# Performance work log

Measured on AMD Instinct MI355X. Metric: run time of the kernel, lower is better.

Reference implementation:

```python
import jax, jax.numpy as jnp
import numpy as np
from jax.scipy.linalg import expm

J = 1.0
TEMP = 2.269
D = 28
RGSTEP = 12
TORDER = (1, 2, 3, 0)


def _plan():
    # statically trace tensor shapes through the RG steps
    shapes, d0s, dcuts = [], [], []
    t = (2, 2, 2, 2)
    for _ in range(RGSTEP):
        n = t[0] * t[0]          # antisymmetric matrix A_i is (n, n)
        dcut = min(D, t[2] * t[2])
        shapes.append(n)
        d0s.append(t[0])
        dcuts.append(dcut)
        # T1 = (dcut, t[1], dcut, t[3]); rotate by (1,2,3,0)
        t = (t[1], dcut, t[3], dcut)
    return shapes, d0s, dcuts

SHAPES, D0S, DCUTS = _plan()
OFFS = np.cumsum([0] + [n * (n - 1) // 2 for n in SHAPES])
TRIU = [np.triu_indices(n, k=1) for n in SHAPES]


def setup_inputs() -> dict:
    key = jax.random.key(0)
    # Ising initial tensor (initT): entries 0.5*sqrt(W_i W_j W_k W_l) for even parity
    beta = -J / TEMP
    W = np.array([np.exp(beta) + np.exp(-beta), np.exp(beta) - np.exp(-beta)])
    idx = np.indices((2, 2, 2, 2))
    par = (idx.sum(0) % 2) == 0
    prod = W[idx[0]] * W[idx[1]] * W[idx[2]] * W[idx[3]]
    T0 = np.where(par, 0.5 * np.sqrt(np.where(par, prod, 1.0)), 0.0)
    Aflat = jax.random.normal(key, (int(OFFS[-1]),), dtype=jnp.float32) * 0.05
    return {"Aflat": Aflat, "T0": jnp.asarray(T0, jnp.float32)}


def _build_Us(Aflat):
    Us = []
    for i in range(RGSTEP):
        n = SHAPES[i]
        seg = Aflat[int(OFFS[i]):int(OFFS[i + 1])]
        r, c = TRIU[i]
        A = jnp.zeros((n, n), Aflat.dtype).at[r, c].set(seg).at[c, r].set(-seg)
        U = expm(A)[:, :DCUTS[i]].reshape(D0S[i], D0S[i], DCUTS[i])
        Us.append(U)
    return Us


def _contract(T, U):
    # T1[a,b,c,e] = sum_{i,j,m,n,p} U[i,j,a] T[i,b,m,n] T[j,n,p,e] U[m,p,c]
    X = jnp.einsum('ija,ibmn->jbmna', U, T)   # O(D^6), peak D^5 intermediate
    Y = jnp.einsum('jbmna,jnpe->bmpea', X, T)  # O(D^7)
    return jnp.einsum('bmpea,mpc->abce', Y, U)  # O(D^6)


def reference(Aflat, T0):
    Us = _build_Us(Aflat)
    T = T0
    fe = jnp.zeros((), T0.dtype)
    for i in range(RGSTEP):
        T1 = _contract(T, Us[i])
        lam = jnp.max(jnp.abs(T1))
        T = jnp.transpose(T1 / lam, TORDER)
        fe = fe - TEMP * jnp.log(lam) / (2.0 ** (i + 1))
    return fe
```

## Files before the change

kernel.cpp:

```cpp
#include <hip/hip_runtime.h>


#define TEMPC 2.269f

typedef unsigned int uint32;
typedef short short8b __attribute__((ext_vector_type(8)));
typedef float f32x4 __attribute__((ext_vector_type(4)));
typedef unsigned short ushort8v __attribute__((ext_vector_type(8)));

__device__ __forceinline__ ushort f2bf(float x) {
  uint32 u = __float_as_uint(x);
  u = (u + 0x7FFFu + ((u >> 16) & 1u)) >> 16;
  return (ushort)u;
}
__device__ __forceinline__ float toF(float x) { return x; }
__device__ __forceinline__ float toF(ushort h) { return __uint_as_float(((uint32)h) << 16); }

__device__ __forceinline__ void gll16(const ushort* g, ushort* l) {
  __builtin_amdgcn_global_load_lds((const __attribute__((address_space(1))) void*)g,
                                   (__attribute__((address_space(3))) void*)l, 16, 0, 0);
}

template<int BM, int BN, bool PD>
__global__ __launch_bounds__(256) void gemm_mfma(
// ... 64 lines not shown
      int rr = li >> 3, ch = li & 7;
      int sch = ch ^ (rr & 7);
      if (isA) {
        if (PD) gll16(A + (long)pdBase[t] + (long)(k0 >> npl) * dsp, &As[tt * 512]);
        else    gll16(Ap + (long)rr * Kp + k0 + sch * 8, &As[tt * 512]);
      } else {
        gll16(Bp + (long)rr * Kp + k0 + sch * 8, &Bs[tt * 512]);
      }
    }
    __syncthreads();
    #pragma unroll
    for (int km = 0; km < 2; ++km) {
      short8b af[FRM], bfv[FRN];
      #pragma unroll
      for (int i = 0; i < FRM; ++i) {
        int rr = wm0 + i * 16 + rl;
        af[i] = *(const short8b*)&As[rr * 64 + ((((km << 2) | cb) ^ (rr & 7)) << 3)];
      }
      #pragma unroll
      for (int j = 0; j < FRN; ++j) {
        int rr = wn0 + j * 16 + rl;
        bfv[j] = *(const short8b*)&Bs[rr * 64 + ((((km << 2) | cb) ^ (rr & 7)) << 3)];
      }
      #pragma unroll
      for (int i = 0; i < FRM; ++i)
        #pragma unroll
        for (int j = 0; j < FRN; ++j)
          acc[i][j] = __builtin_amdgcn_mfma_f32_16x16x32_bf16(af[i], bfv[j], acc[i][j], 0, 0, 0);
    }
    __syncthreads();
  }
  const int r4 = (lane >> 4) * 4, cl = lane & 15;
  #pragma unroll
  for (int i = 0; i < FRM; ++i) {
    #pragma unroll
    for (int j = 0; j < FRN; ++j) {
      int row0 = m0 + wm0 + i * 16 + r4;
      int col  = n0 + wn0 + j * 16 + cl;
      #pragma unroll
      for (int qq = 0; qq < 4; ++qq) {
        long off2 = (long)bz * sC + (long)(row0 + qq) * Np + col;
        float v = acc[i][j][qq];
        if (mode & 1) v += cA * Aadd[off2] + ((row0 + qq) == col ? cI : 0.0f);
        if (mode & 2) Cf[off2] = v;
        if (mode & 4) Cb[off2] = f2bf(v);
      }
    }
  }
}

template<typename TI>
__global__ __launch_bounds__(256) void trans_to_bfT(const TI* __restrict__ in, ushort* __restrict__ out,
                                                    int R, int C, int inStride, int outStride, int Rpad,
                                                    long sIn, long sOut)
{
  __shared__ float sm[32][33];
  const TI* ip = in + (long)blockIdx.z * sIn;
  ushort* op = out + (long)blockIdx.z * sOut;
  int c0 = blockIdx.x * 32, r0 = blockIdx.y * 32;
  int lx = threadIdx.x & 31, ly = threadIdx.x >> 5;
  #pragma unroll
  for (int yy = 0; yy < 4; ++yy) {
    int r = r0 + ly + yy * 8, c = c0 + lx;
    if (r < R && c < C) sm[ly + yy * 8][lx] = toF(ip[(long)r * inStride + c]);
  }
  __syncthreads();
  #pragma unroll
  for (int yy = 0; yy < 4; ++yy) {
    int orow = c0 + ly + yy * 8;
    int ocol = r0 + lx;
    if (orow < C && ocol < Rpad) {
      ushort v = 0;
      if (ocol < R) v = f2bf(sm[lx][ly + yy * 8]);
      op[(long)orow * outStride + ocol] = v;
    }
  }
}

template<typename TT>
__global__ __launch_bounds__(256) void transTk2(const TT* __restrict__ T, ushort* __restrict__ out,
                                                int d0, int t3, int npl, long R1, long R1p)
{
  long idx = (long)blockIdx.x * 256 + threadIdx.x;
  if (idx >= R1p * 64) return;
  long rp = idx >> 6; int ii = (int)(idx & 63);
  long bm = rp >> npl; int n = (int)(rp & ((1 << npl) - 1));
  ushort v = 0;
  if (ii < d0 && n < t3) v = f2bf(toF(T[(long)ii * R1 + bm * t3 + n]));
  out[idx] = v;
}

template<typename TI>
__global__ __launch_bounds__(256) void build_B2(const TI* __restrict__ in, ushort* __restrict__ out,
                                                int t2, int t3, int d0, int npl, int Kp2, int Nr)
{
  __shared__ float sm[32][33];
  const int npad = 1 << npl;
  int oc0 = blockIdx.x * 32, or0 = blockIdx.y * 32;
  int lx = threadIdx.x & 31, ly = threadIdx.x >> 5;
  #pragma unroll
  for (int yy = 0; yy < 4; ++yy) {
    int ocol = oc0 + ly + yy * 8;
    int orow = or0 + lx;
    float v = 0.f;
    int j = ocol >> npl, n = ocol & (npad - 1);
    if (n < t3 && orow < Nr && j < d0) {
      int p = orow / t3, e = orow - p * t3;
      v = toF(in[((long)(j * t3 + n) * t2 + p) * t3 + e]);
    }
    sm[ly + yy * 8][lx] = v;
  }
  __syncthreads();
  #pragma unroll
  for (int yy = 0; yy < 4; ++yy) {
    int orow = or0 + ly + yy * 8;
    int ocol = oc0 + lx;
    if (orow < Nr) out[(long)orow * Kp2 + ocol] = f2bf(sm[lx][ly + yy * 8]);
  }
}

__global__ __launch_bounds__(256) void build_ut1(const float* __restrict__ U, ushort* __restrict__ out,
                                                 int d0, int dc, int Mpad, long uStr, long oStr)
{
  const int bt = blockIdx.y;
  int idx = blockIdx.x * 256 + threadIdx.x;
  if (idx >= Mpad * 64) return;
  int ja = idx >> 6, ii = idx & 63;
  ushort v = 0;
  if (ii < d0 && ja < d0 * dc) {
    int j = ja / dc, a = ja - j * dc;
    v = f2bf(U[bt * uStr + ((long)ii * d0 + j) * dc + a]);
  }
  out[bt * oStr + idx] = v;
}

__global__ __launch_bounds__(256) void build_ut3(const float* __restrict__ U, ushort* __restrict__ out,
                                                 int d0, int dc, int Kp3, long uStr, long oStr)
{
  const int bt = blockIdx.y;
  int idx = blockIdx.x * 256 + threadIdx.x;
  if (idx >= 64 * Kp3) return;
  int c = idx / Kp3, mp = idx - c * Kp3;
  ushort v = 0;
  if (c < dc && mp < d0 * d0) v = f2bf(U[bt * uStr + (long)mp * dc + c]);
  out[bt * oStr + idx] = v;
}

template<int KPG>
__global__ __launch_bounds__(256) void k3_fused(
    const ushort* __restrict__ Y, const ushort* __restrict__ Ut3,
    float* __restrict__ Z2, unsigned* __restrict__ lamslot,
    int d0, int t2, int t3, int dc, int NpY)
{
  __shared__ __align__(16) ushort sYt[32 * KPG];
  const int tid = threadIdx.x;
  const int wid = tid >> 6, lane = tid & 63;
  const int b = blockIdx.x / dc, a = blockIdx.x - b * dc;
  for (int i8 = tid; i8 < 32 * KPG / 8; i8 += 256) *(ushort8v*)&sYt[i8 * 8] = ushort8v{};
  __syncthreads();
  const int nv = NpY / 8;
  for (int idx = tid; idx < t2 * nv; idx += 256) {
    int m = idx / nv, v = idx - m * nv;
    int col0 = v * 8;
    ushort8v val = *(const ushort8v*)(Y + ((long)(b * t2 + m) * dc + a) * NpY + col0);
    #pragma unroll
    for (int u = 0; u < 8; ++u) {
      int col = col0 + u;
      int p = (t3 == 16) ? (col >> 4) : ((col * 9363) >> 18);
      if (p < t2) {
        int e = col - p * t3;
        int k = m * d0 + p;
        sYt[e * KPG + ((((k >> 3) ^ (e & 7)) << 3) | (k & 7))] = val[u];
      }
    }
  }
  __syncthreads();
  const int kpw = KPG / 4, k0w = wid * kpw;
  const int rl = lane & 15, cb = lane >> 4;
  f32x4 acc[2][2];
  #pragma unroll
  for (int i = 0; i < 2; ++i)
    #pragma unroll
    for (int j = 0; j < 2; ++j) { acc[i][j][0]=0.f; acc[i][j][1]=0.f; acc[i][j][2]=0.f; acc[i][j][3]=0.f; }
  for (int kk = 0; kk < kpw; kk += 32) {
    int kb = k0w + kk + cb * 8;
    short8b af[2], bfv[2];
    #pragma unroll
    for (int i = 0; i < 2; ++i) {
      int e = i * 16 + rl;
      af[i] = *(const short8b*)&sYt[e * KPG + (((kb >> 3) ^ (e & 7)) << 3)];
      bfv[i] = *(const short8b*)(Ut3 + (long)(i * 16 + rl) * KPG + kb);
    }
    #pragma unroll
    for (int i = 0; i < 2; ++i)
      #pragma unroll
      for (int j = 0; j < 2; ++j)
        acc[i][j] = __builtin_amdgcn_mfma_f32_16x16x32_bf16(af[i], bfv[j], acc[i][j], 0, 0, 0);
  }
  __syncthreads();
  float* Lp = (float*)sYt;
  #pragma unroll
  for (int i = 0; i < 2; ++i)
    #pragma unroll
    for (int j = 0; j < 2; ++j)
      #pragma unroll
      for (int qq = 0; qq < 4; ++qq) {
        int e32 = i * 16 + (lane >> 4) * 4 + qq;
        int c32 = j * 16 + (lane & 15);
        Lp[wid * 1024 + e32 * 32 + c32] = acc[i][j][qq];
      }
  __syncthreads();
  float mx = 0.f;
  for (int idx = tid; idx < 1024; idx += 256) {
    float z = Lp[idx] + Lp[1024 + idx] + Lp[2048 + idx] + Lp[3072 + idx];
    int e = idx >> 5, c = idx & 31;
    if (e < t3 && c < dc) {
      Z2[((long)(b * dc + a) * t3 + e) * 64 + c] = z;
      mx = fmaxf(mx, fabsf(z));
    }
  }
  __syncthreads();
  Lp[tid] = mx;
  __syncthreads();
  for (int s = 128; s > 0; s >>= 1) {
    if (tid < s) Lp[tid] = fmaxf(Lp[tid], Lp[tid + s]);
    __syncthreads();
  }
  if (tid == 0) atomicMax(lamslot, __float_as_uint(Lp[0]));
}

__global__ __launch_bounds__(256) void permute_scale2d(const float* __restrict__ Z2, ushort* __restrict__ Tn,
                                                       const unsigned* __restrict__ lamslot,
                                                       float* __restrict__ fe, float w, float* __restrict__ dout,
                                                       int dc, int t3)
{
  extern __shared__ char dynC[];
  ushort* sm = (ushort*)dynC;
  const int b = blockIdx.x;
  const int c0 = blockIdx.y * 7;
  const int tid = threadIdx.x;
  const float lam = __uint_as_float(*lamslot);
  const float s = 1.0f / lam;
  if (b == 0 && blockIdx.y == 0 && tid == 0) {
    float f = fe[0] - w * logf(lam);
    fe[0] = f; dout[0] = f;
  }
  const int TD = t3 * dc;
  const int tot = dc * t3 * 7;
  for (int idx = tid; idx < tot; idx += 256) {
    int c7 = idx % 7; int rm = idx / 7;
    int e = rm % t3; int a = rm / t3;
    float v = Z2[(((long)(b * dc + a)) * t3 + e) * 64 + c0 + c7] * s;
    sm[(c7 * t3 + e) * dc + a] = f2bf(v);
  }
  __syncthreads();
  const long ob = (long)(b * dc + c0) * TD;
  for (int idx = tid; idx < tot / 8; idx += 256)
    *(ushort8v*)(Tn + ob + idx * 8) = *(ushort8v*)(sm + idx * 8);
}

__global__ __launch_bounds__(256) void build_A2(const float* __restrict__ Aflat, float* __restrict__ Af,
                                                ushort* __restrict__ Ab, ushort* __restrict__ An,
                                                int n, int Np, long aoff, long tri, float sc)
{
  const int b = blockIdx.y;
  const long nn = (long)Np * Np;
  const long id = (long)blockIdx.x * 256 + threadIdx.x;
  if (id >= nn) return;
  const int r = (int)(id / Np), c = (int)(id % Np);
  float v = 0.0f;
  if (r < n && c < n) {
    if (c > r)      v =  Aflat[aoff + b * tri + (long)r * (n - 1) - (long)r * (r - 1) / 2 + (c - r - 1)] * sc;
    else if (c < r) v = -Aflat[aoff + b * tri + (long)c * (n - 1) - (long)c * (c - 1) / 2 + (r - c - 1)] * sc;
  }
  long o = b * nn + id;
  Af[o] = v; Ab[o] = f2bf(v); An[o] = f2bf(-v);
}

__global__ __launch_bounds__(256) void axpy_q2(const ushort* __restrict__ A2b, const float* __restrict__ Af,
                                               ushort* __restrict__ Qb, int Np)
{
  const int b = blockIdx.y;
  const long nn = (long)Np * Np;
  const long id = (long)blockIdx.x * 256 + threadIdx.x;
  if (id >= nn) return;
  const int r = (int)(id / Np), c = (int)(id % Np);
  long o = b * nn + id;
  float v = (1.0f/40320.0f) * toF(A2b[o]) + (1.0f/5040.0f) * Af[o] + ((r == c) ? (1.0f/720.0f) : 0.0f);
  Qb[o] = f2bf(v);
}

__global__ __launch_bounds__(256) void extract_u2(const float* __restrict__ E, float* __restrict__ W,
                                                  int n, int dcut, int rowStride, long ubase, long ustride, long estride)
{
  const int b = blockIdx.y;
  const long tot = (long)n * dcut;
  const long id = (long)blockIdx.x * 256 + threadIdx.x;
  if (id >= tot) return;
  const int rr = (int)(id / dcut), aa = (int)(id % dcut);
  W[ubase + b * ustride + id] = E[b * estride + (long)rr * rowStride + aa];
}

struct SmallStep { int n, d0, dcut, s; long aoff; long uoff; };
struct SmallStep4 { SmallStep st[4]; };

__global__ __launch_bounds__(256) void expm_small_kernel(const float* __restrict__ Aflat,
                                                         float* __restrict__ W, SmallStep4 ps)
{
  SmallStep p = ps.st[blockIdx.x];
  const int n = p.n, nn = n * n;
  __shared__ float As[256], A2[256], Qa[256], Qb[256];
  const int tid = threadIdx.x;
  const int r = (tid < nn) ? (tid / n) : 0;
  const int c = (tid < nn) ? (tid % n) : 0;
  const float sc = 1.0f / (float)(1 << p.s);
  if (tid < nn) {
    float v = 0.0f;
    if (c > r)      v =  Aflat[p.aoff + (long)r*(n-1) - (long)r*(r-1)/2 + (c - r - 1)] * sc;
    else if (c < r) v = -Aflat[p.aoff + (long)c*(n-1) - (long)c*(c-1)/2 + (r - c - 1)] * sc;
    As[tid] = v;
  }
  __syncthreads();
  if (tid < nn) {
    float s2 = 0.0f;
    for (int k = 0; k < n; ++k) s2 += As[r*n+k] * As[k*n+c];
    A2[tid] = s2;
  }
  __syncthreads();
  if (tid < nn)
    Qa[tid] = (1.0f/40320.0f)*A2[tid] + (1.0f/5040.0f)*As[tid] + ((r==c) ? (1.0f/720.0f) : 0.0f);
  __syncthreads();
  float* qp = Qa; float* qn = Qb;
  const float cis[3] = {1.0f/24.0f, 0.5f, 1.0f};
  const float cas[3] = {1.0f/120.0f, 1.0f/6.0f, 1.0f};
  #pragma unroll
  for (int it = 0; it < 3; ++it) {
    if (tid < nn) {
      float s2 = 0.0f;
      for (int k = 0; k < n; ++k) s2 += A2[r*n+k] * qp[k*n+c];
      qn[tid] = s2 + cas[it]*As[tid] + ((r==c) ? cis[it] : 0.0f);
    }
    __syncthreads();
    float* t = qp; qp = qn; qn = t;
  }
  for (int it = 0; it < p.s; ++it) {
    float s2 = 0.0f;
    if (tid < nn) { for (int k = 0; k < n; ++k) s2 += qp[r*n+k] * qp[k*n+c]; }
    if (tid < nn) qn[tid] = s2;
    __syncthreads();
    float* t = qp; qp = qn; qn = t;
  }
  if (tid < n * p.dcut) {
    int rr = tid / p.dcut, aa = tid % p.dcut;
    W[p.uoff + tid] = qp[rr*n + aa];
  }
}

template<int BM, int BN, int BK, int TM, int TN>
__global__ __launch_bounds__(256) void gemm_f32(
    const float* __restrict__ A, const float* __restrict__ B, float* __restrict__ C,
    int M, int N, int K)
{
  constexpr int PAD = 4;
  __shared__ float As[BK][BM + PAD];
  __shared__ float Bs[BK][BN + PAD];
  const int tid = threadIdx.x;
  const int m0 = blockIdx.y * BM, n0 = blockIdx.x * BN;
  constexpr int TX = BN / TN;
  const int tx = tid % TX, ty = tid / TX;
  float acc[TM][TN];
  #pragma unroll
  for (int i = 0; i < TM; ++i)
    #pragma unroll
    for (int j = 0; j < TN; ++j) acc[i][j] = 0.0f;

  const int a_m = tid / (BK / 4);
  const int a_k = (tid % (BK / 4)) * 4;
  const int b_k = tid / (BN / 4);
  const int b_n = (tid % (BN / 4)) * 4;

  for (int k0 = 0; k0 < K; k0 += BK) {
    float4 av = make_float4(0.f, 0.f, 0.f, 0.f);
    if (m0 + a_m < M && k0 + a_k < K)
      av = *(const float4*)(A + (long)(m0 + a_m) * K + k0 + a_k);
    As[a_k + 0][a_m] = av.x; As[a_k + 1][a_m] = av.y;
    As[a_k + 2][a_m] = av.z; As[a_k + 3][a_m] = av.w;
    float4 bv = make_float4(0.f, 0.f, 0.f, 0.f);
    if (k0 + b_k < K && n0 + b_n < N)
      bv = *(const float4*)(B + (long)(k0 + b_k) * N + n0 + b_n);
    *(float4*)&Bs[b_k][b_n] = bv;
    __syncthreads();
    #pragma unroll
    for (int kk = 0; kk < BK; ++kk) {
      float af[TM], bf[TN];
      #pragma unroll
      for (int i = 0; i < TM; i += 4) *(float4*)&af[i] = *(const float4*)&As[kk][ty*TM + i];
      #pragma unroll
      for (int j = 0; j < TN; j += 4) *(float4*)&bf[j] = *(const float4*)&Bs[kk][tx*TN + j];
      #pragma unroll
      for (int i = 0; i < TM; ++i)
        #pragma unroll
        for (int j = 0; j < TN; ++j)
          acc[i][j] = fmaf(af[i], bf[j], acc[i][j]);
    }
    __syncthreads();
  }
  #pragma unroll
  for (int i = 0; i < TM; ++i) {
    int row = m0 + ty*TM + i;
    if (row >= M) continue;
    #pragma unroll
    for (int j = 0; j < TN; ++j) {
      int col = n0 + tx*TN + j;
      if (col >= N) continue;
      C[(long)row * N + col] = acc[i][j];
    }
  }
}

__global__ __launch_bounds__(256) void k1_kernel2(const float* __restrict__ T, const float* __restrict__ U,
                                                  float* __restrict__ X2f,
                                                  int t1, int t2, int t3, int d0, int dcut, int K)
{
  extern __shared__ char dyn3[];
  float* lds = (float*)dyn3;
  float* Ts = lds;
  float* Us = lds + d0 * t3;
  const int tid = threadIdx.x;
  const int bm = blockIdx.x;
  const long tstride = (long)t1 * t2 * t3;
  const long tbase = (long)bm * t3;
  for (int idx = tid; idx < d0 * t3; idx += 256) {
    int i = idx / t3, nn = idx % t3;
    Ts[idx] = T[(long)i * tstride + tbase + nn];
  }
  const int nout = dcut * t3;
  __syncthreads();
  for (int j = 0; j < d0; ++j) {
    for (int idx = tid; idx < d0 * dcut; idx += 256)
      Us[idx] = U[((long)(idx / dcut) * d0 + j) * dcut + (idx % dcut)];
    __syncthreads();
    for (int idx = tid; idx < nout; idx += 256) {
      int a = idx / t3, nn = idx % t3;
      float s = 0.0f;
      for (int i = 0; i < d0; ++i) s += Ts[i*t3 + nn] * Us[i*dcut + a];
      X2f[((long)bm * dcut + a) * K + j * t3 + nn] = s;
    }
    __syncthreads();
  }
}

__global__ __launch_bounds__(256) void k3_kernel2(const float* __restrict__ Y, const float* __restrict__ U,
                                                  float* __restrict__ Z, int t1, int t2, int t3, int d0, int dcut,
                                                  int Ystride)
{
  extern __shared__ char dyn4[];
  float* lds = (float*)dyn4;
  float* Ys = lds;
  float* Us = lds + d0 * t3;
  const int tid = threadIdx.x;
  const int ba = blockIdx.x;
  const int b = ba / dcut, a = ba % dcut;
  const int nout = dcut * t3;
  float acc[4] = {0.f, 0.f, 0.f, 0.f};
  for (int m = 0; m < t2; ++m) {
    const long yrow = ((long)(b*t2 + m) * dcut + a) * Ystride;
    for (int idx = tid; idx < d0 * t3; idx += 256) Ys[idx] = Y[yrow + idx];
    for (int idx = tid; idx < d0 * dcut; idx += 256) Us[idx] = U[(long)m * d0 * dcut + idx];
    __syncthreads();
    #pragma unroll
    for (int o = 0; o < 4; ++o) {
      int idx = tid + o * 256;
      if (idx < nout) {
        int cc = idx / t3, e = idx % t3;
        float s = 0.0f;
        for (int p = 0; p < d0; ++p) s += Ys[p*t3 + e] * Us[p*dcut + cc];
        acc[o] += s;
      }
    }
    __syncthreads();
  }
  #pragma unroll
  for (int o = 0; o < 4; ++o) {
    int idx = tid + o * 256;
    if (idx < nout) {
      int cc = idx / t3, e = idx % t3;
      Z[(((long)a * t1 + b) * dcut + cc) * t3 + e] = acc[o];
    }
  }
}

__global__ __launch_bounds__(256) void redmax1_kernel(const float* __restrict__ Z, long cnt, float* __restrict__ part)
{
  __shared__ float sm[256];
  float v = 0.0f;
  for (long i = (long)blockIdx.x * 256 + threadIdx.x; i < cnt; i += (long)gridDim.x * 256)
    v = fmaxf(v, fabsf(Z[i]));
  sm[threadIdx.x] = v; __syncthreads();
  for (int s = 128; s > 0; s >>= 1) {
    if ((int)threadIdx.x < s) sm[threadIdx.x] = fmaxf(sm[threadIdx.x], sm[threadIdx.x + s]);
    __syncthreads();
  }
  if (threadIdx.x == 0) part[blockIdx.x] = sm[0];
}

__global__ __launch_bounds__(256) void redmax2_kernel(const float* __restrict__ part, float* __restrict__ invlam,
                                                      float* __restrict__ fe, float w, float* __restrict__ dout)
{
  __shared__ float sm[256];
  sm[threadIdx.x] = part[threadIdx.x]; __syncthreads();
  for (int s = 128; s > 0; s >>= 1) {
    if ((int)threadIdx.x < s) sm[threadIdx.x] = fmaxf(sm[threadIdx.x], sm[threadIdx.x + s]);
    __syncthreads();
  }
  if (threadIdx.x == 0) {
    float lam = sm[0];
    invlam[0] = 1.0f / lam;
    float f = fe[0] - w * logf(lam);
    fe[0] = f;
    dout[0] = f;
  }
}

__global__ __launch_bounds__(256) void permute_scale_kernel(const float* __restrict__ Z, float* __restrict__ Tn,
                                                            const float* __restrict__ invlam, int t1, int t3, int dcut)
{
  extern __shared__ char dyn5[];
  float* lds = (float*)dyn5;
  const int tid = threadIdx.x;
  const int bc = blockIdx.x;
  const int b = bc / dcut, c = bc % dcut;
  const float s = invlam[0];
  const int tot = dcut * t3;
  for (int idx = tid; idx < tot; idx += 256) {
    int a = idx / t3, e = idx % t3;
    lds[idx] = Z[(((long)a * t1 + b) * dcut + c) * t3 + e] * s;
  }
  __syncthreads();
  const long ob = (long)bc * t3 * dcut;
  for (int idx = tid; idx < tot; idx += 256) {
    int e = idx / dcut, a = idx % dcut;
    Tn[ob + idx] = lds[a * t3 + e];
  }
}

__global__ void init_kernel(const float* __restrict__ T0, float* __restrict__ Tdst, float* __restrict__ W)
{
  int t = threadIdx.x;
  if (t < 16) Tdst[t] = T0[t];
  if (t == 0) W[0] = 0.0f;
  if (t >= 8 && t < 20) ((unsigned*)W)[t] = 0u;
}

extern "C" void kernel_launch(void* const* d_in, const int* in_sizes, int n_in,
                              void* d_out, int out_size, void* d_ws, size_t ws_size,
                              hipStream_t stream)
{
  const float* Aflat = (const float*)d_in[0];
  const float* T0    = (const float*)d_in[1];
  float* out = (float*)d_out;
  float* W = (float*)d_ws;
  (void)ws_size; (void)in_sizes; (void)n_in; (void)out_size;

  const int SH_n[12]  = {4,4,16,16,256,256,784,784,784,784,784,784};
  const int SH_d0[12] = {2,2,4,4,16,16,28,28,28,28,28,28};
  const int SH_dc[12] = {4,4,16,16,28,28,28,28,28,28,28,28};
  long aoff[12]; { long o = 0; for (int i = 0; i < 12; ++i) { aoff[i] = o; o += (long)SH_n[i]*(SH_n[i]-1)/2; } }
  long uoff[12]; { long o = 1024; for (int i = 0; i < 12; ++i) { uoff[i] = o; o += (long)SH_d0[i]*SH_d0[i]*SH_dc[i]; } }
  int T1d[12], T2d[12], T3d[12], T0d[12];
  { int a=2,b=2,c=2,d=2;
    for (int i = 0; i < 12; ++i) { T0d[i]=a; T1d[i]=b; T2d[i]=c; T3d[i]=d;
      int dc = SH_dc[i]; int na=b, nb=dc, nc=d, nd=dc; a=na; b=nb; c=nc; d=nd; } }

  const long FE = 0, INVLAM = 1, LAMV = 8, PART = 64;
  const long TA   = 150016;
  const long TB   = TA + 614656;
  const long Z2o  = TB + 614656;
  const long TTK  = Z2o + 1409024;
  const long TTo  = TTK + 802816;
  const long UT1o = TTo + 401408;
  const long UT3o = UT1o + 212992;
  const long BIG0 = UT3o + 229376;
  const long BIG2 = BIG0 + 10500000;
  const long X2F  = BIG2 + 9863168;
  const long YFo  = X2F + 100000;
  const long P_Af  = BIG0;
  const long P_S4  = BIG0 + 4816896;
  const long P_bf  = BIG0 + 5200000;
  const long P_Ab  = P_bf;
  const long P_An  = P_bf + 2408448;
  const long P_A2b = P_bf + 2*2408448;
  const long P_Q0  = P_bf + 3*2408448;
  const long P_Q1  = P_bf + 4*2408448;
  const long P_QT  = P_bf + 5*2408448;
  const long P_Bb  = BIG0 + 19700000;
  const long B_Af  = P_Bb;
  const long B_S4  = P_Bb + 131072;
  const long B_Ab  = P_Bb + 163840;
  const long B_An  = B_Ab + 65536;
  const long B_A2b = B_An + 65536;
  const long B_Q0  = B_A2b + 65536;
  const long B_Q1  = B_Q0 + 65536;
  const long B_QT  = B_Q1 + 65536;

  const float c5 = 1.0f/120.0f, c4 = 1.0f/24.0f, c3 = 1.0f/6.0f, c2 = 0.5f;

  ushort* TTKp = (ushort*)(W + TTK);
  ushort* B2b  = (ushort*)(W + TTo);
  ushort* UT1p = (ushort*)(W + UT1o);
  ushort* UT3p = (ushort*)(W + UT3o);
  ushort* Pb   = (ushort*)(W + BIG0);
  ushort* Yb   = (ushort*)(W + BIG2);
  float*  X2F_ = W + X2F;
  float*  YF_  = W + YFo;
  float*  Z2f  = W + Z2o;
  unsigned* lamV = (unsigned*)(W + LAMV);

  {
    SmallStep4 sp;
    const int ss[4] = {0,0,1,1};
    for (int i = 0; i < 4; ++i) {
      sp.st[i].n = SH_n[i]; sp.st[i].d0 = SH_d0[i]; sp.st[i].dcut = SH_dc[i];
      sp.st[i].s = ss[i]; sp.st[i].aoff = aoff[i]; sp.st[i].uoff = uoff[i];
    }
    expm_small_kernel<<<4, 256, 0, stream>>>(Aflat, W, sp);
  }

  {
    const int n = 784, Np = 896, bt = 6;
    const long NN = (long)Np * Np;
    float* Af = W + P_Af;  float* S4 = W + P_S4;
    ushort* Ab = (ushort*)(W + P_Ab);  ushort* An = (ushort*)(W + P_An);
    ushort* A2b = (ushort*)(W + P_A2b);
    ushort* Q0 = (ushort*)(W + P_Q0);  ushort* Q1 = (ushort*)(W + P_Q1);
    ushort* QT = (ushort*)(W + P_QT);
    dim3 ge((int)((NN + 255) / 256), bt);
    build_A2<<<ge, 256, 0, stream>>>(Aflat, Af, Ab, An, n, Np, aoff[6], 306936, 0.25f);
    dim3 g(Np/128, Np/128, bt);
    dim3 gt(Np/32, Np/32, bt);
    gemm_mfma<128,128,false><<<g,256,0,stream>>>(Ab, An, nullptr, A2b, nullptr, 0.f, 0.f, 4, Np, Np, NN, NN, NN, 0,0,1);
    axpy_q2<<<ge, 256, 0, stream>>>(A2b, Af, Q0, Np);
    gemm_mfma<128,128,false><<<g,256,0,stream>>>(Q0, A2b, nullptr, Q1, Af, c5, c4, 5, Np, Np, NN, NN, NN, 0,0,1);
    gemm_mfma<128,128,false><<<g,256,0,stream>>>(Q1, A2b, nullptr, Q0, Af, c3, c2, 5, Np, Np, NN, NN, NN, 0,0,1);
    gemm_mfma<128,128,false><<<g,256,0,stream>>>(Q0, A2b, nullptr, Q1, Af, 1.f, 1.f, 5, Np, Np, NN, NN, NN, 0,0,1);
    trans_to_bfT<ushort><<<gt,256,0,stream>>>(Q1, QT, Np, Np, Np, Np, Np, NN, NN);
    gemm_mfma<128,128,false><<<g,256,0,stream>>>(Q1, QT, nullptr, Q0, nullptr, 0.f, 0.f, 4, Np, Np, NN, NN, NN, 0,0,1);
    trans_to_bfT<ushort><<<dim3(2, Np/32, bt),256,0,stream>>>(Q0, QT, Np, 64, Np, Np, Np, NN, NN);
    gemm_mfma<64,64,false><<<dim3(1, Np/64, bt),256,0,stream>>>(Q0, QT, S4, nullptr, nullptr, 0.f, 0.f, 2,
                                                                64, Np, NN, NN, 57344, 0,0,1);
    extract_u2<<<dim3(86, bt), 256, 0, stream>>>(S4, W, n, 28, 64, uoff[6], 21952, 57344);
  }

  {
    const int n = 256, Np = 256, bt = 2;
    const long NN = (long)Np * Np;
    float* Af = W + B_Af;  float* S4 = W + B_S4;
    ushort* Ab = (ushort*)(W + B_Ab);  ushort* An = (ushort*)(W + B_An);
    ushort* A2b = (ushort*)(W + B_A2b);
    ushort* Q0 = (ushort*)(W + B_Q0);  ushort* Q1 = (ushort*)(W + B_Q1);
    ushort* QT = (ushort*)(W + B_QT);
    dim3 ge((int)((NN + 255) / 256), bt);
    build_A2<<<ge, 256, 0, stream>>>(Aflat, Af, Ab, An, n, Np, aoff[4], 32640, 0.25f);
    dim3 g(Np/128, Np/128, bt);
    dim3 gt(Np/32, Np/32, bt);
    gemm_mfma<128,128,false><<<g,256,0,stream>>>(Ab, An, nullptr, A2b, nullptr, 0.f, 0.f, 4, Np, Np, NN, NN, NN, 0,0,1);
    axpy_q2<<<ge, 256, 0, stream>>>(A2b, Af, Q0, Np);
    gemm_mfma<128,128,false><<<g,256,0,stream>>>(Q0, A2b, nullptr, Q1, Af, c5, c4, 5, Np, Np, NN, NN, NN, 0,0,1);
    gemm_mfma<128,128,false><<<g,256,0,stream>>>(Q1, A2b, nullptr, Q0, Af, c3, c2, 5, Np, Np, NN, NN, NN, 0,0,1);
    gemm_mfma<128,128,false><<<g,256,0,stream>>>(Q0, A2b, nullptr, Q1, Af, 1.f, 1.f, 5, Np, Np, NN, NN, NN, 0,0,1);
    trans_to_bfT<ushort><<<gt,256,0,stream>>>(Q1, QT, Np, Np, Np, Np, Np, NN, NN);
    gemm_mfma<128,128,false><<<g,256,0,stream>>>(Q1, QT, nullptr, Q0, nullptr, 0.f, 0.f, 4, Np, Np, NN, NN, NN, 0,0,1);
    trans_to_bfT<ushort><<<dim3(2, Np/32, bt),256,0,stream>>>(Q0, QT, Np, 64, Np, Np, Np, NN, NN);
    gemm_mfma<64,64,false><<<dim3(1, Np/64, bt),256,0,stream>>>(Q0, QT, S4, nullptr, nullptr, 0.f, 0.f, 2,
                                                                64, Np, NN, NN, 16384, 0,0,1);
    extract_u2<<<dim3(28, bt), 256, 0, stream>>>(S4, W, n, 28, 64, uoff[4], 7168, 16384);
  }

  build_ut1<<<dim3(208, 2), 256, 0, stream>>>(W + uoff[4], UT1p, 16, 28, 832, 7168, 832*64);
  build_ut1<<<dim3(208, 6), 256, 0, stream>>>(W + uoff[6], UT1p + 2L*832*64, 28, 28, 832, 21952, 832*64);
  build_ut3<<<dim3(64, 2), 256, 0, stream>>>(W + uoff[4], UT3p, 16, 28, 256, 7168, 64*896);
  build_ut3<<<dim3(224, 6), 256, 0, stream>>>(W + uoff[6], UT3p + 2L*64*896, 28, 28, 896, 21952, 64*896);

  float* Tcur = W + TA;
  float* Tnext = W + TB;
  init_kernel<<<1, 256, 0, stream>>>(T0, Tcur, W);

  for (int i = 0; i < 12; ++i) {
    const int t1 = T1d[i], t2 = T2d[i], t3 = T3d[i], d0 = T0d[i], dc = SH_dc[i];
    const float* U = W + uoff[i];
    const int M = t1*t2*dc, K = d0*t3, N = t2*t3;
    const float w = TEMPC / (float)(1 << (i + 1));

    if (i < 4) {
      const int lds1 = (d0*t3 + d0*dc) * (int)sizeof(float);
      k1_kernel2<<<t1*t2, 256, lds1, stream>>>(Tcur, U, X2F_, t1, t2, t3, d0, dc, K);
      dim3 g2((N + 127) / 128, (M + 127) / 128, 1);
      gemm_f32<128,128,8,8,8><<<g2, 256, 0, stream>>>(X2F_, Tcur, YF_, M, N, K);
      const int lds3 = (d0*t3 + d0*dc) * (int)sizeof(float);
      k3_kernel2<<<t1*dc, 256, lds3, stream>>>(YF_, U, Z2f, t1, t2, t3, d0, dc, N);
      const long redCnt = (long)dc * t1 * dc * t3;
      redmax1_kernel<<<256, 256, 0, stream>>>(Z2f, redCnt, W + PART);
      redmax2_kernel<<<1, 256, 0, stream>>>(W + PART, W + INVLAM, W + FE, w, out);
      permute_scale_kernel<<<t1*dc, 256, dc*t3*(int)sizeof(float), stream>>>(
          Z2f, Tnext, W + INVLAM, t1, t3, dc);
    } else {
      const bool inBf = (i >= 5);
      const int npl = (t3 == 16) ? 4 : 5;
      const int npad = 1 << npl;
      const int Kp2 = d0 * npad;
      const int Npd = (N + 127) / 128 * 128;
      const long R1 = (long)t1 * t2 * t3;
      const long R1p = (long)t1 * t2 * npad;
      const int Mpad1 = (d0*dc + 63)/64*64;
      const int Mpad2 = (M + 127)/128*128;
      const ushort* Ut1_i = UT1p + (long)(i-4)*832*64;
      const ushort* Ut3_i = UT3p + (long)(i-4)*64*896;
      unsigned* lam_i = lamV + (i - 4);

      if (inBf) transTk2<ushort><<<(int)((R1p*64 + 255)/256), 256, 0, stream>>>(
          (const ushort*)Tcur, TTKp, d0, t3, npl, R1, R1p);
      else      transTk2<float><<<(int)((R1p*64 + 255)/256), 256, 0, stream>>>(
          Tcur, TTKp, d0, t3, npl, R1, R1p);
      gemm_mfma<64,64,false><<<dim3((int)(R1p/64), Mpad1/64), 256, 0, stream>>>(
          Ut1_i, TTKp, nullptr, Pb, nullptr, 0.f, 0.f, 4, (int)R1p, 64, 0, 0, 0, 0, 0, 1);

      if (inBf) build_B2<ushort><<<dim3(Kp2/32, (N + 31)/32), 256, 0, stream>>>(
          (const ushort*)Tcur, B2b, t2, t3, d0, npl, Kp2, N);
      else      build_B2<float><<<dim3(Kp2/32, (N + 31)/32), 256, 0, stream>>>(
          Tcur, B2b, t2, t3, d0, npl, Kp2, N);
      gemm_mfma<128,128,true><<<dim3(Npd/128, Mpad2/128), 256, 0, stream>>>(
          Pb, B2b, nullptr, Yb, nullptr, 0.f, 0.f, 4, Npd, Kp2, 0, 0, 0,
          (int)R1p, npl, dc);

      if (d0 == 16) k3_fused<256><<<t1*dc, 256, 0, stream>>>(Yb, Ut3_i, Z2f, lam_i, d0, t2, t3, dc, Npd);
      else          k3_fused<896><<<t1*dc, 256, 0, stream>>>(Yb, Ut3_i, Z2f, lam_i, d0, t2, t3, dc, Npd);
      permute_scale2d<<<dim3(t1, 4), 256, 7*t3*dc*2, stream>>>(
          Z2f, (ushort*)Tnext, lam_i, W + FE, w, out, dc, t3);
    }

    float* tmp = Tcur; Tcur = Tnext; Tnext = tmp;
  }
}
```

Baseline: 1.249 ms.

## Fuse first three RG steps into one block, route step 3 through MFMA path, cut expm squaring

```diff
diff --git a/kernel.cpp b/kernel.cpp
--- a/kernel.cpp
+++ b/kernel.cpp
@@ -240,7 +240,8 @@
     float* __restrict__ Z2, unsigned* __restrict__ lamslot,
     int d0, int t2, int t3, int dc, int NpY)
 {
-  __shared__ __align__(16) ushort sYt[32 * KPG];
+  constexpr int LDSN = (32 * KPG < 8192) ? 8192 : 32 * KPG;
+  __shared__ __align__(16) ushort sYt[LDSN];
   const int tid = threadIdx.x;
   const int wid = tid >> 6, lane = tid & 63;
   const int b = blockIdx.x / dc, a = blockIdx.x - b * dc;
@@ -320,12 +321,12 @@
 __global__ __launch_bounds__(256) void permute_scale2d(const float* __restrict__ Z2, ushort* __restrict__ Tn,
                                                        const unsigned* __restrict__ lamslot,
                                                        float* __restrict__ fe, float w, float* __restrict__ dout,
-                                                       int dc, int t3)
+                                                       int dc, int t3, int chunk)
 {
   extern __shared__ char dynC[];
   ushort* sm = (ushort*)dynC;
   const int b = blockIdx.x;
-  const int c0 = blockIdx.y * 7;
+  const int c0 = blockIdx.y * chunk;
   const int tid = threadIdx.x;
   const float lam = __uint_as_float(*lamslot);
   const float s = 1.0f / lam;
@@ -334,9 +335,9 @@
     fe[0] = f; dout[0] = f;
   }
   const int TD = t3 * dc;
-  const int tot = dc * t3 * 7;
+  const int tot = dc * t3 * chunk;
   for (int idx = tid; idx < tot; idx += 256) {
-    int c7 = idx % 7; int rm = idx / 7;
+    int c7 = idx % chunk; int rm = idx / chunk;
     int e = rm % t3; int a = rm / t3;
     float v = Z2[(((long)(b * dc + a)) * t3 + e) * 64 + c0 + c7] * s;
     sm[(c7 * t3 + e) * dc + a] = f2bf(v);
@@ -444,198 +445,78 @@
   }
 }
 
-template<int BM, int BN, int BK, int TM, int TN>
-__global__ __launch_bounds__(256) void gemm_f32(
-    const float* __restrict__ A, const float* __restrict__ B, float* __restrict__ C,
-    int M, int N, int K)
-{
-  constexpr int PAD = 4;
-  __shared__ float As[BK][BM + PAD];
-  __shared__ float Bs[BK][BN + PAD];
+__global__ __launch_bounds__(256) void small_steps_kernel(
+    const float* __restrict__ T0in, const float* __restrict__ Wu,
+    long u0, long u1, long u2, float* __restrict__ Tout, float* __restrict__ fe)
+{
+  __shared__ float Tb[256], X2[4096], Yb[4096], Zb[4096], red[256];
   const int tid = threadIdx.x;
-  const int m0 = blockIdx.y * BM, n0 = blockIdx.x * BN;
-  constexpr int TX = BN / TN;
-  const int tx = tid % TX, ty = tid / TX;
-  float acc[TM][TN];
-  #pragma unroll
-  for (int i = 0; i < TM; ++i)
-    #pragma unroll
-    for (int j = 0; j < TN; ++j) acc[i][j] = 0.0f;
-
-  const int a_m = tid / (BK / 4);
-  const int a_k = (tid % (BK / 4)) * 4;
-  const int b_k = tid / (BN / 4);
-  const int b_n = (tid % (BN / 4)) * 4;
-
-  for (int k0 = 0; k0 < K; k0 += BK) {
-    float4 av = make_float4(0.f, 0.f, 0.f, 0.f);
-    if (m0 + a_m < M && k0 + a_k < K)
-      av = *(const float4*)(A + (long)(m0 + a_m) * K + k0 + a_k);
-    As[a_k + 0][a_m] = av.x; As[a_k + 1][a_m] = av.y;
-    As[a_k + 2][a_m] = av.z; As[a_k + 3][a_m] = av.w;
-    float4 bv = make_float4(0.f, 0.f, 0.f, 0.f);
-    if (k0 + b_k < K && n0 + b_n < N)
-      bv = *(const float4*)(B + (long)(k0 + b_k) * N + n0 + b_n);
-    *(float4*)&Bs[b_k][b_n] = bv;
-    __syncthreads();
-    #pragma unroll
-    for (int kk = 0; kk < BK; ++kk) {
-      float af[TM], bf[TN];
-      #pragma unroll
-      for (int i = 0; i < TM; i += 4) *(float4*)&af[i] = *(const float4*)&As[kk][ty*TM + i];
-      #pragma unroll
-      for (int j = 0; j < TN; j += 4) *(float4*)&bf[j] = *(const float4*)&Bs[kk][tx*TN + j];
-      #pragma unroll
-      for (int i = 0; i < TM; ++i)
-        #pragma unroll
-        for (int j = 0; j < TN; ++j)
-          acc[i][j] = fmaf(af[i], bf[j], acc[i][j]);
-    }
-    __syncthreads();
-  }
-  #pragma unroll
-  for (int i = 0; i < TM; ++i) {
-    int row = m0 + ty*TM + i;
-    if (row >= M) continue;
-    #pragma unroll
-    for (int j = 0; j < TN; ++j) {
-      int col = n0 + tx*TN + j;
-      if (col >= N) continue;
-      C[(long)row * N + col] = acc[i][j];
-    }
-  }
-}
-
-__global__ __launch_bounds__(256) void k1_kernel2(const float* __restrict__ T, const float* __restrict__ U,
-                                                  float* __restrict__ X2f,
-                                                  int t1, int t2, int t3, int d0, int dcut, int K)
-{
-  extern __shared__ char dyn3[];
-  float* lds = (float*)dyn3;
-  float* Ts = lds;
-  float* Us = lds + d0 * t3;
-  const int tid = threadIdx.x;
-  const int bm = blockIdx.x;
-  const long tstride = (long)t1 * t2 * t3;
-  const long tbase = (long)bm * t3;
-  for (int idx = tid; idx < d0 * t3; idx += 256) {
-    int i = idx / t3, nn = idx % t3;
-    Ts[idx] = T[(long)i * tstride + tbase + nn];
-  }
-  const int nout = dcut * t3;
-  __syncthreads();
-  for (int j = 0; j < d0; ++j) {
-    for (int idx = tid; idx < d0 * dcut; idx += 256)
-      Us[idx] = U[((long)(idx / dcut) * d0 + j) * dcut + (idx % dcut)];
-    __syncthreads();
-    for (int idx = tid; idx < nout; idx += 256) {
-      int a = idx / t3, nn = idx % t3;
-      float s = 0.0f;
-      for (int i = 0; i < d0; ++i) s += Ts[i*t3 + nn] * Us[i*dcut + a];
-      X2f[((long)bm * dcut + a) * K + j * t3 + nn] = s;
-    }
-    __syncthreads();
-  }
-}
-
-__global__ __launch_bounds__(256) void k3_kernel2(const float* __restrict__ Y, const float* __restrict__ U,
-                                                  float* __restrict__ Z, int t1, int t2, int t3, int d0, int dcut,
-                                                  int Ystride)
-{
-  extern __shared__ char dyn4[];
-  float* lds = (float*)dyn4;
-  float* Ys = lds;
-  float* Us = lds + d0 * t3;
-  const int tid = threadIdx.x;
-  const int ba = blockIdx.x;
-  const int b = ba / dcut, a = ba % dcut;
-  const int nout = dcut * t3;
-  float acc[4] = {0.f, 0.f, 0.f, 0.f};
-  for (int m = 0; m < t2; ++m) {
-    const long yrow = ((long)(b*t2 + m) * dcut + a) * Ystride;
-    for (int idx = tid; idx < d0 * t3; idx += 256) Ys[idx] = Y[yrow + idx];
-    for (int idx = tid; idx < d0 * dcut; idx += 256) Us[idx] = U[(long)m * d0 * dcut + idx];
-    __syncthreads();
-    #pragma unroll
-    for (int o = 0; o < 4; ++o) {
-      int idx = tid + o * 256;
-      if (idx < nout) {
-        int cc = idx / t3, e = idx % t3;
-        float s = 0.0f;
-        for (int p = 0; p < d0; ++p) s += Ys[p*t3 + e] * Us[p*dcut + cc];
-        acc[o] += s;
-      }
-    }
-    __syncthreads();
-  }
-  #pragma unroll
-  for (int o = 0; o < 4; ++o) {
-    int idx = tid + o * 256;
-    if (idx < nout) {
-      int cc = idx / t3, e = idx % t3;
-      Z[(((long)a * t1 + b) * dcut + cc) * t3 + e] = acc[o];
-    }
-  }
-}
-
-__global__ __launch_bounds__(256) void redmax1_kernel(const float* __restrict__ Z, long cnt, float* __restrict__ part)
-{
-  __shared__ float sm[256];
-  float v = 0.0f;
-  for (long i = (long)blockIdx.x * 256 + threadIdx.x; i < cnt; i += (long)gridDim.x * 256)
-    v = fmaxf(v, fabsf(Z[i]));
-  sm[threadIdx.x] = v; __syncthreads();
-  for (int s = 128; s > 0; s >>= 1) {
-    if ((int)threadIdx.x < s) sm[threadIdx.x] = fmaxf(sm[threadIdx.x], sm[threadIdx.x + s]);
-    __syncthreads();
-  }
-  if (threadIdx.x == 0) part[blockIdx.x] = sm[0];
-}
-
-__global__ __launch_bounds__(256) void redmax2_kernel(const float* __restrict__ part, float* __restrict__ invlam,
-                                                      float* __restrict__ fe, float w, float* __restrict__ dout)
-{
-  __shared__ float sm[256];
-  sm[threadIdx.x] = part[threadIdx.x]; __syncthreads();
-  for (int s = 128; s > 0; s >>= 1) {
-    if ((int)threadIdx.x < s) sm[threadIdx.x] = fmaxf(sm[threadIdx.x], sm[threadIdx.x + s]);
-    __syncthreads();
-  }
-  if (threadIdx.x == 0) {
-    float lam = sm[0];
-    invlam[0] = 1.0f / lam;
-    float f = fe[0] - w * logf(lam);
-    fe[0] = f;
-    dout[0] = f;
-  }
-}
-
-__global__ __launch_bounds__(256) void permute_scale_kernel(const float* __restrict__ Z, float* __restrict__ Tn,
-                                                            const float* __restrict__ invlam, int t1, int t3, int dcut)
-{
-  extern __shared__ char dyn5[];
-  float* lds = (float*)dyn5;
-  const int tid = threadIdx.x;
-  const int bc = blockIdx.x;
-  const int b = bc / dcut, c = bc % dcut;
-  const float s = invlam[0];
-  const int tot = dcut * t3;
-  for (int idx = tid; idx < tot; idx += 256) {
-    int a = idx / t3, e = idx % t3;
-    lds[idx] = Z[(((long)a * t1 + b) * dcut + c) * t3 + e] * s;
-  }
-  __syncthreads();
-  const long ob = (long)bc * t3 * dcut;
-  for (int idx = tid; idx < tot; idx += 256) {
-    int e = idx / dcut, a = idx % dcut;
-    Tn[ob + idx] = lds[a * t3 + e];
-  }
-}
-
-__global__ void init_kernel(const float* __restrict__ T0, float* __restrict__ Tdst, float* __restrict__ W)
+  const int D0[3]={2,2,4}, Tt1[3]={2,4,4}, Tt2[3]={2,2,4}, Tt3[3]={2,4,4}, DCv[3]={4,4,16};
+  const long UO[3]={u0,u1,u2};
+  if (tid < 16) Tb[tid] = T0in[tid];
+  float feacc = 0.0f;
+  __syncthreads();
+  for (int st = 0; st < 3; ++st) {
+    const int d0=D0[st], t1=Tt1[st], t2=Tt2[st], t3=Tt3[st], dc=DCv[st];
+    const int M = t1*t2*dc, K = d0*t3, N = t2*t3;
+    const int R = t1*t2*t3;
+    const float* U = Wu + UO[st];
+    for (int idx = tid; idx < M*K; idx += 256) {
+      int row = idx / K, k = idx - row*K;
+      int bm = row / dc, a = row - bm*dc;
+      int j = k / t3, n = k - j*t3;
+      float s = 0.f;
+      for (int i2 = 0; i2 < d0; ++i2)
+        s += Tb[i2*R + bm*t3 + n] * U[(i2*d0 + j)*dc + a];
+      X2[idx] = s;
+    }
+    __syncthreads();
+    for (int idx = tid; idx < M*N; idx += 256) {
+      int row = idx / N, col = idx - row*N;
+      float s = 0.f;
+      for (int k = 0; k < K; ++k) s += X2[row*K + k] * Tb[k*N + col];
+      Yb[idx] = s;
+    }
+    __syncthreads();
+    const int ZS = dc*t1*dc*t3;
+    for (int idx = tid; idx < ZS; idx += 256) {
+      int e = idx % t3; int r2 = idx / t3;
+      int c = r2 % dc; int r3 = r2 / dc;
+      int b = r3 % t1; int a = r3 / t1;
+      float s = 0.f;
+      for (int m = 0; m < t2; ++m)
+        for (int p = 0; p < t2; ++p)
+          s += Yb[((b*t2 + m)*dc + a)*N + p*t3 + e] * U[(m*d0 + p)*dc + c];
+      Zb[idx] = s;
+    }
+    __syncthreads();
+    float mx = 0.f;
+    for (int idx = tid; idx < ZS; idx += 256) mx = fmaxf(mx, fabsf(Zb[idx]));
+    red[tid] = mx; __syncthreads();
+    for (int s2 = 128; s2 > 0; s2 >>= 1) {
+      if (tid < s2) red[tid] = fmaxf(red[tid], red[tid + s2]);
+      __syncthreads();
+    }
+    float lam = red[0];
+    feacc -= (TEMPC / (float)(1 << (st + 1))) * logf(lam);
+    float inv = 1.0f / lam;
+    __syncthreads();
+    const int TS = t1*dc*t3*dc;
+    for (int idx = tid; idx < TS; idx += 256) {
+      int a = idx % dc; int r2 = idx / dc;
+      int e = r2 % t3; int r3 = r2 / t3;
+      int c = r3 % dc; int b = r3 / dc;
+      float v = Zb[(((long)a*t1 + b)*dc + c)*t3 + e] * inv;
+      if (st == 2) Tout[idx] = v; else Tb[idx] = v;
+    }
+    __syncthreads();
+  }
+  if (tid == 0) fe[0] = feacc;
+}
+
+__global__ void init_kernel(float* __restrict__ W)
 {
   int t = threadIdx.x;
-  if (t < 16) Tdst[t] = T0[t];
   if (t == 0) W[0] = 0.0f;
   if (t >= 8 && t < 20) ((unsigned*)W)[t] = 0u;
 }
@@ -660,18 +541,16 @@
     for (int i = 0; i < 12; ++i) { T0d[i]=a; T1d[i]=b; T2d[i]=c; T3d[i]=d;
       int dc = SH_dc[i]; int na=b, nb=dc, nc=d, nd=dc; a=na; b=nb; c=nc; d=nd; } }
 
-  const long FE = 0, INVLAM = 1, LAMV = 8, PART = 64;
+  const long FE = 0, LAMV = 8;
   const long TA   = 150016;
   const long TB   = TA + 614656;
   const long Z2o  = TB + 614656;
   const long TTK  = Z2o + 1409024;
   const long TTo  = TTK + 802816;
   const long UT1o = TTo + 401408;
-  const long UT3o = UT1o + 212992;
-  const long BIG0 = UT3o + 229376;
+  const long UT3o = UT1o + 240000;
+  const long BIG0 = UT3o + 258048;
   const long BIG2 = BIG0 + 10500000;
-  const long X2F  = BIG2 + 9863168;
-  const long YFo  = X2F + 100000;
   const long P_Af  = BIG0;
   const long P_S4  = BIG0 + 4816896;
   const long P_bf  = BIG0 + 5200000;
@@ -699,8 +578,6 @@
   ushort* UT3p = (ushort*)(W + UT3o);
   ushort* Pb   = (ushort*)(W + BIG0);
   ushort* Yb   = (ushort*)(W + BIG2);
-  float*  X2F_ = W + X2F;
-  float*  YF_  = W + YFo;
   float*  Z2f  = W + Z2o;
   unsigned* lamV = (unsigned*)(W + LAMV);
 
@@ -723,18 +600,15 @@
     ushort* Q0 = (ushort*)(W + P_Q0);  ushort* Q1 = (ushort*)(W + P_Q1);
     ushort* QT = (ushort*)(W + P_QT);
     dim3 ge((int)((NN + 255) / 256), bt);
-    build_A2<<<ge, 256, 0, stream>>>(Aflat, Af, Ab, An, n, Np, aoff[6], 306936, 0.25f);
+    build_A2<<<ge, 256, 0, stream>>>(Aflat, Af, Ab, An, n, Np, aoff[6], 306936, 0.5f);
     dim3 g(Np/128, Np/128, bt);
-    dim3 gt(Np/32, Np/32, bt);
     gemm_mfma<128,128,false><<<g,256,0,stream>>>(Ab, An, nullptr, A2b, nullptr, 0.f, 0.f, 4, Np, Np, NN, NN, NN, 0,0,1);
     axpy_q2<<<ge, 256, 0, stream>>>(A2b, Af, Q0, Np);
     gemm_mfma<128,128,false><<<g,256,0,stream>>>(Q0, A2b, nullptr, Q1, Af, c5, c4, 5, Np, Np, NN, NN, NN, 0,0,1);
     gemm_mfma<128,128,false><<<g,256,0,stream>>>(Q1, A2b, nullptr, Q0, Af, c3, c2, 5, Np, Np, NN, NN, NN, 0,0,1);
     gemm_mfma<128,128,false><<<g,256,0,stream>>>(Q0, A2b, nullptr, Q1, Af, 1.f, 1.f, 5, Np, Np, NN, NN, NN, 0,0,1);
-    trans_to_bfT<ushort><<<gt,256,0,stream>>>(Q1, QT, Np, Np, Np, Np, Np, NN, NN);
-    gemm_mfma<128,128,false><<<g,256,0,stream>>>(Q1, QT, nullptr, Q0, nullptr, 0.f, 0.f, 4, Np, Np, NN, NN, NN, 0,0,1);
-    trans_to_bfT<ushort><<<dim3(2, Np/32, bt),256,0,stream>>>(Q0, QT, Np, 64, Np, Np, Np, NN, NN);
-    gemm_mfma<64,64,false><<<dim3(1, Np/64, bt),256,0,stream>>>(Q0, QT, S4, nullptr, nullptr, 0.f, 0.f, 2,
+    trans_to_bfT<ushort><<<dim3(2, Np/32, bt),256,0,stream>>>(Q1, QT, Np, 64, Np, Np, Np, NN, NN);
+    gemm_mfma<64,64,false><<<dim3(1, Np/64, bt),256,0,stream>>>(Q1, QT, S4, nullptr, nullptr, 0.f, 0.f, 2,
                                                                 64, Np, NN, NN, 57344, 0,0,1);
     extract_u2<<<dim3(86, bt), 256, 0, stream>>>(S4, W, n, 28, 64, uoff[6], 21952, 57344);
   }
@@ -748,83 +622,69 @@
     ushort* Q0 = (ushort*)(W + B_Q0);  ushort* Q1 = (ushort*)(W + B_Q1);
     ushort* QT = (ushort*)(W + B_QT);
     dim3 ge((int)((NN + 255) / 256), bt);
-    build_A2<<<ge, 256, 0, stream>>>(Aflat, Af, Ab, An, n, Np, aoff[4], 32640, 0.25f);
+    build_A2<<<ge, 256, 0, stream>>>(Aflat, Af, Ab, An, n, Np, aoff[4], 32640, 0.5f);
     dim3 g(Np/128, Np/128, bt);
-    dim3 gt(Np/32, Np/32, bt);
     gemm_mfma<128,128,false><<<g,256,0,stream>>>(Ab, An, nullptr, A2b, nullptr, 0.f, 0.f, 4, Np, Np, NN, NN, NN, 0,0,1);
     axpy_q2<<<ge, 256, 0, stream>>>(A2b, Af, Q0, Np);
     gemm_mfma<128,128,false><<<g,256,0,stream>>>(Q0, A2b, nullptr, Q1, Af, c5, c4, 5, Np, Np, NN, NN, NN, 0,0,1);
     gemm_mfma<128,128,false><<<g,256,0,stream>>>(Q1, A2b, nullptr, Q0, Af, c3, c2, 5, Np, Np, NN, NN, NN, 0,0,1);
     gemm_mfma<128,128,false><<<g,256,0,stream>>>(Q0, A2b, nullptr, Q1, Af, 1.f, 1.f, 5, Np, Np, NN, NN, NN, 0,0,1);
-    trans_to_bfT<ushort><<<gt,256,0,stream>>>(Q1, QT, Np, Np, Np, Np, Np, NN, NN);
-    gemm_mfma<128,128,false><<<g,256,0,stream>>>(Q1, QT, nullptr, Q0, nullptr, 0.f, 0.f, 4, Np, Np, NN, NN, NN, 0,0,1);
-    trans_to_bfT<ushort><<<dim3(2, Np/32, bt),256,0,stream>>>(Q0, QT, Np, 64, Np, Np, Np, NN, NN);
-    gemm_mfma<64,64,false><<<dim3(1, Np/64, bt),256,0,stream>>>(Q0, QT, S4, nullptr, nullptr, 0.f, 0.f, 2,
+    trans_to_bfT<ushort><<<dim3(2, Np/32, bt),256,0,stream>>>(Q1, QT, Np, 64, Np, Np, Np, NN, NN);
+    gemm_mfma<64,64,false><<<dim3(1, Np/64, bt),256,0,stream>>>(Q1, QT, S4, nullptr, nullptr, 0.f, 0.f, 2,
                                                                 64, Np, NN, NN, 16384, 0,0,1);
     extract_u2<<<dim3(28, bt), 256, 0, stream>>>(S4, W, n, 28, 64, uoff[4], 7168, 16384);
   }
 
-  build_ut1<<<dim3(208, 2), 256, 0, stream>>>(W + uoff[4], UT1p, 16, 28, 832, 7168, 832*64);
-  build_ut1<<<dim3(208, 6), 256, 0, stream>>>(W + uoff[6], UT1p + 2L*832*64, 28, 28, 832, 21952, 832*64);
-  build_ut3<<<dim3(64, 2), 256, 0, stream>>>(W + uoff[4], UT3p, 16, 28, 256, 7168, 64*896);
-  build_ut3<<<dim3(224, 6), 256, 0, stream>>>(W + uoff[6], UT3p + 2L*64*896, 28, 28, 896, 21952, 64*896);
-
+  build_ut1<<<dim3(16, 1), 256, 0, stream>>>(W + uoff[3], UT1p, 4, 16, 64, 0, 0);
+  build_ut3<<<dim3(32, 1), 256, 0, stream>>>(W + uoff[3], UT3p, 4, 16, 128, 0, 0);
+  build_ut1<<<dim3(112, 2), 256, 0, stream>>>(W + uoff[4], UT1p + 1L*832*64, 16, 28, 448, 7168, 832*64);
+  build_ut3<<<dim3(64, 2), 256, 0, stream>>>(W + uoff[4], UT3p + 1L*64*896, 16, 28, 256, 7168, 64*896);
+  build_ut1<<<dim3(208, 6), 256, 0, stream>>>(W + uoff[6], UT1p + 3L*832*64, 28, 28, 832, 21952, 832*64);
+  build_ut3<<<dim3(224, 6), 256, 0, stream>>>(W + uoff[6], UT3p + 3L*64*896, 28, 28, 896, 21952, 64*896);
+
+  init_kernel<<<1, 64, 0, stream>>>(W);
   float* Tcur = W + TA;
   float* Tnext = W + TB;
-  init_kernel<<<1, 256, 0, stream>>>(T0, Tcur, W);
-
-  for (int i = 0; i < 12; ++i) {
+  small_steps_kernel<<<1, 256, 0, stream>>>(T0, W, uoff[0], uoff[1], uoff[2], Tcur, W + FE);
+
+  for (int i = 3; i < 12; ++i) {
     const int t1 = T1d[i], t2 = T2d[i], t3 = T3d[i], d0 = T0d[i], dc = SH_dc[i];
-    const float* U = W + uoff[i];
-    const int M = t1*t2*dc, K = d0*t3, N = t2*t3;
+    const int M = t1*t2*dc, N = t2*t3;
     const float w = TEMPC / (float)(1 << (i + 1));
-
-    if (i < 4) {
-      const int lds1 = (d0*t3 + d0*dc) * (int)sizeof(float);
-      k1_kernel2<<<t1*t2, 256, lds1, stream>>>(Tcur, U, X2F_, t1, t2, t3, d0, dc, K);
-      dim3 g2((N + 127) / 128, (M + 127) / 128, 1);
-      gemm_f32<128,128,8,8,8><<<g2, 256, 0, stream>>>(X2F_, Tcur, YF_, M, N, K);
-      const int lds3 = (d0*t3 + d0*dc) * (int)sizeof(float);
-      k3_kernel2<<<t1*dc, 256, lds3, stream>>>(YF_, U, Z2f, t1, t2, t3, d0, dc, N);
-      const long redCnt = (long)dc * t1 * dc * t3;
-      redmax1_kernel<<<256, 256, 0, stream>>>(Z2f, redCnt, W + PART);
-      redmax2_kernel<<<1, 256, 0, stream>>>(W + PART, W + INVLAM, W + FE, w, out);
-      permute_scale_kernel<<<t1*dc, 256, dc*t3*(int)sizeof(float), stream>>>(
-          Z2f, Tnext, W + INVLAM, t1, t3, dc);
-    } else {
-      const bool inBf = (i >= 5);
-      const int npl = (t3 == 16) ? 4 : 5;
-      const int npad = 1 << npl;
-      const int Kp2 = d0 * npad;
-      const int Npd = (N + 127) / 128 * 128;
-      const long R1 = (long)t1 * t2 * t3;
-      const long R1p = (long)t1 * t2 * npad;
-      const int Mpad1 = (d0*dc + 63)/64*64;
-      const int Mpad2 = (M + 127)/128*128;
-      const ushort* Ut1_i = UT1p + (long)(i-4)*832*64;
-      const ushort* Ut3_i = UT3p + (long)(i-4)*64*896;
-      unsigned* lam_i = lamV + (i - 4);
-
-      if (inBf) transTk2<ushort><<<(int)((R1p*64 + 255)/256), 256, 0, stream>>>(
-          (const ushort*)Tcur, TTKp, d0, t3, npl, R1, R1p);
-      else      transTk2<float><<<(int)((R1p*64 + 255)/256), 256, 0, stream>>>(
-          Tcur, TTKp, d0, t3, npl, R1, R1p);
-      gemm_mfma<64,64,false><<<dim3((int)(R1p/64), Mpad1/64), 256, 0, stream>>>(
-          Ut1_i, TTKp, nullptr, Pb, nullptr, 0.f, 0.f, 4, (int)R1p, 64, 0, 0, 0, 0, 0, 1);
-
-      if (inBf) build_B2<ushort><<<dim3(Kp2/32, (N + 31)/32), 256, 0, stream>>>(
-          (const ushort*)Tcur, B2b, t2, t3, d0, npl, Kp2, N);
-      else      build_B2<float><<<dim3(Kp2/32, (N + 31)/32), 256, 0, stream>>>(
-          Tcur, B2b, t2, t3, d0, npl, Kp2, N);
-      gemm_mfma<128,128,true><<<dim3(Npd/128, Mpad2/128), 256, 0, stream>>>(
-          Pb, B2b, nullptr, Yb, nullptr, 0.f, 0.f, 4, Npd, Kp2, 0, 0, 0,
-          (int)R1p, npl, dc);
-
-      if (d0 == 16) k3_fused<256><<<t1*dc, 256, 0, stream>>>(Yb, Ut3_i, Z2f, lam_i, d0, t2, t3, dc, Npd);
-      else          k3_fused<896><<<t1*dc, 256, 0, stream>>>(Yb, Ut3_i, Z2f, lam_i, d0, t2, t3, dc, Npd);
-      permute_scale2d<<<dim3(t1, 4), 256, 7*t3*dc*2, stream>>>(
-          Z2f, (ushort*)Tnext, lam_i, W + FE, w, out, dc, t3);
-    }
+    const bool inBf = (i >= 4);
+    const int npl = (t3 == 16) ? 4 : 5;
+    const int npad = 1 << npl;
+    const int Kp2 = d0 * npad;
+    const int Npd = (N + 127) / 128 * 128;
+    const long R1 = (long)t1 * t2 * t3;
+    const long R1p = (long)t1 * t2 * npad;
+    const int Mpad1 = (d0*dc + 63)/64*64;
+    const int Mpad2 = (M + 127)/128*128;
+    const ushort* Ut1_i = UT1p + (long)(i-3)*832*64;
+    const ushort* Ut3_i = UT3p + (long)(i-3)*64*896;
+    unsigned* lam_i = lamV + (i - 3);
+
+    if (inBf) transTk2<ushort><<<(int)((R1p*64 + 255)/256), 256, 0, stream>>>(
+        (const ushort*)Tcur, TTKp, d0, t3, npl, R1, R1p);
+    else      transTk2<float><<<(int)((R1p*64 + 255)/256), 256, 0, stream>>>(
+        Tcur, TTKp, d0, t3, npl, R1, R1p);
+    gemm_mfma<64,64,false><<<dim3((int)(R1p/64), Mpad1/64), 256, 0, stream>>>(
+        Ut1_i, TTKp, nullptr, Pb, nullptr, 0.f, 0.f, 4, (int)R1p, 64, 0, 0, 0, 0, 0, 1);
+
+    if (inBf) build_B2<ushort><<<dim3(Kp2/32, (N + 31)/32), 256, 0, stream>>>(
+        (const ushort*)Tcur, B2b, t2, t3, d0, npl, Kp2, N);
+    else      build_B2<float><<<dim3(Kp2/32, (N + 31)/32), 256, 0, stream>>>(
+        Tcur, B2b, t2, t3, d0, npl, Kp2, N);
+    gemm_mfma<128,128,true><<<dim3(Npd/128, Mpad2/128), 256, 0, stream>>>(
+        Pb, B2b, nullptr, Yb, nullptr, 0.f, 0.f, 4, Npd, Kp2, 0, 0, 0,
+        (int)R1p, npl, dc);
+
+    if (d0 == 4)       k3_fused<128><<<t1*dc, 256, 0, stream>>>(Yb, Ut3_i, Z2f, lam_i, d0, t2, t3, dc, Npd);
+    else if (d0 == 16) k3_fused<256><<<t1*dc, 256, 0, stream>>>(Yb, Ut3_i, Z2f, lam_i, d0, t2, t3, dc, Npd);
+    else               k3_fused<896><<<t1*dc, 256, 0, stream>>>(Yb, Ut3_i, Z2f, lam_i, d0, t2, t3, dc, Npd);
+    const int chunk = (dc == 16) ? 4 : 7;
+    permute_scale2d<<<dim3(t1, dc/chunk), 256, chunk*t3*dc*2, stream>>>(
+        Z2f, (ushort*)Tnext, lam_i, W + FE, w, out, dc, t3, chunk);
 
     float* tmp = Tcur; Tcur = Tnext; Tnext = tmp;
   }
```

Result: faster. 1.181 ms (-5.4%).
